# Optimization experiments

Hardware: AMD Instinct MI355X
Metric: run time of the kernel (lower is better)

## Reference

```python
import jax, jax.numpy as jnp
import numpy as np

DIM = 768
NUM_HEADS = 12
HEAD_DIM = DIM // NUM_HEADS
SCALE = HEAD_DIM ** -0.5


def setup_inputs() -> dict:
    key = jax.random.key(0)
    k_x, k_qw, k_qb, k_pw, k_pb = jax.random.split(key, 5)
    B, S = 4, 2048
    x = jax.random.normal(k_x, (B, S, DIM), dtype=jnp.float32)
    # torch nn.Linear convention: weight shape [out_features, in_features]
    qkv_w = jax.random.normal(k_qw, (2 * DIM, DIM), dtype=jnp.float32) * 0.02
    qkv_b = jax.random.normal(k_qb, (2 * DIM,), dtype=jnp.float32) * 0.02
    proj_w = jax.random.normal(k_pw, (DIM, DIM), dtype=jnp.float32) * 0.02
    proj_b = jax.random.normal(k_pb, (DIM,), dtype=jnp.float32) * 0.02
    return {"x": x, "qkv_w": qkv_w, "qkv_b": qkv_b, "proj_w": proj_w, "proj_b": proj_b}


def reference(x, qkv_w, qkv_b, proj_w, proj_b):
    B, S, D = x.shape
    H, Hd = NUM_HEADS, HEAD_DIM
    # qkv projection -> (B, S, 2*D)
    qkv = jnp.einsum('bsd,ed->bse', x, qkv_w) + qkv_b
    # reshape to (B, S, 2, H, Hd) then split q, v with heads leading: (B, H, S, Hd)
    qkv = qkv.reshape(B, S, 2, H, Hd).transpose(2, 0, 3, 1, 4)
    q, v = qkv[0], qkv[1]
    q = q * SCALE
    # shared Q=K scores: (B, H, S, S)
    attn = jnp.einsum('bhid,bhjd->bhij', q, q)
    attn = jax.nn.softmax(attn, axis=-1)  # attn_drop p=0 (identity)
    out = jnp.einsum('bhij,bhjd->bhid', attn, v)
    out = out.transpose(0, 2, 1, 3).reshape(B, S, D)
    out = jnp.einsum('bsd,ed->bse', out, proj_w) + proj_b  # proj_drop p=0
    return out
```

## Files before the change

kernel.cpp:

```cpp
#include <hip/hip_runtime.h>
#include <hip/hip_bf16.h>

#define NH 12
#define HD 64
#define SEQ 2048
#define DM 768

typedef __attribute__((ext_vector_type(8))) short bf16x8;
typedef __attribute__((ext_vector_type(4))) short bf16x4;
typedef __attribute__((ext_vector_type(4))) float f32x4;

static __device__ __forceinline__ unsigned short f2bf(float f) {
  unsigned int u = __float_as_uint(f);
  u += 0x7fff + ((u >> 16) & 1);
  return (unsigned short)(u >> 16);
}

static __device__ __forceinline__ unsigned cvt_pk_bf16(float lo, float hi) {
  unsigned r;
  asm("v_cvt_pk_bf16_f32 %0, %1, %2" : "=v"(r) : "v"(lo), "v"(hi));
  return r;
}

static __device__ __forceinline__ void gload_lds16(const void* g, void* l) {
  __builtin_amdgcn_global_load_lds(
      (const __attribute__((address_space(1))) void*)g,
      (__attribute__((address_space(3))) void*)l, 16, 0, 0);
}

#define QSCALE 0.15014030f

__global__ __launch_bounds__(256) void cvt3_kernel(
    const float* __restrict__ s0, unsigned short* __restrict__ d0, int n0,
    const float* __restrict__ s1, unsigned short* __restrict__ d1, int n1,
    const float* __restrict__ s2, unsigned short* __restrict__ d2, int n2) {
  int i = blockIdx.x * 256 + threadIdx.x;
  const int stride = gridDim.x * 256;
  const int ntot = n0 + n1 + n2;
  for (; i < ntot; i += stride) {
    const float* src;
    unsigned short* dst;
    int j = i;
    if (j < n0) { src = s0; dst = d0; }
    else if (j < n0 + n1) { j -= n0; src = s1; dst = d1; }
    else { j -= n0 + n1; src = s2; dst = d2; }
    const float4 a = reinterpret_cast<const float4*>(src)[j * 2];
    const float4 b = reinterpret_cast<const float4*>(src)[j * 2 + 1];
    ushort4 lo = make_ushort4(f2bf(a.x), f2bf(a.y), f2bf(a.z), f2bf(a.w));
    ushort4 hi = make_ushort4(f2bf(b.x), f2bf(b.y), f2bf(b.z), f2bf(b.w));
    reinterpret_cast<ushort4*>(dst)[j * 2] = lo;
    reinterpret_cast<ushort4*>(dst)[j * 2 + 1] = hi;
  }
}

__global__ __launch_bounds__(256) void qkv_kernel(
    const unsigned short* __restrict__ xb, const unsigned short* __restrict__ wb,
    const float* __restrict__ bias,
    unsigned short* __restrict__ qb, unsigned short* __restrict__ vtb) {
  __shared__ alignas(16) char As[2][8192];
  __shared__ alignas(16) char Bs[2][8192];
  const int tid = threadIdx.x;
  const int lane = tid & 63, wid = tid >> 6;
  const int wr = wid >> 1, wc = wid & 1;
  const int g = lane >> 4, c = lane & 15;
  const int m0 = blockIdx.x * 128, n0 = blockIdx.y * 128;
  const char* Ab = (const char*)xb;
  const char* Bb = (const char*)wb;

  const int o0 = tid * 16, o1 = tid * 16 + 4096;
  const int r0 = o0 >> 6, r1 = o1 >> 6;
  const int sw0 = (o0 & 63) ^ (((r0 >> 1) & 3) << 4);
  const int sw1 = (o1 & 63) ^ (((r1 >> 1) & 3) << 4);

  auto stage = [&](int kt, int buf) {
    const int k0b = kt * 64;
    gload_lds16(Ab + (size_t)(m0 + r0) * 1536 + k0b + sw0, &As[buf][o0]);
    gload_lds16(Bb + (size_t)(n0 + r0) * 1536 + k0b + sw0, &Bs[buf][o0]);
    gload_lds16(Ab + (size_t)(m0 + r1) * 1536 + k0b + sw1, &As[buf][o1]);
    gload_lds16(Bb + (size_t)(n0 + r1) * 1536 + k0b + sw1, &Bs[buf][o1]);
  };

  f32x4 acc[4][4] = {};
  stage(0, 0);

  for (int kt = 0; kt < 24; ++kt) {
    __syncthreads();
    if (kt < 23) stage(kt + 1, (kt + 1) & 1);
    const char* Ap = As[kt & 1];
    const char* Bp = Bs[kt & 1];
    bf16x8 a_f[4], b_f[4];
#pragma unroll
    for (int i = 0; i < 4; ++i) {
      const int ra = wr * 64 + i * 16 + c;
      const int rb = wc * 64 + i * 16 + c;
      a_f[i] = *reinterpret_cast<const bf16x8*>(Ap + ra * 64 + ((g ^ ((ra >> 1) & 3)) << 4));
      b_f[i] = *reinterpret_cast<const bf16x8*>(Bp + rb * 64 + ((g ^ ((rb >> 1) & 3)) << 4));
    }
#pragma unroll
    for (int ai = 0; ai < 4; ++ai)
#pragma unroll
      for (int ni = 0; ni < 4; ++ni)
        acc[ai][ni] = __builtin_amdgcn_mfma_f32_16x16x32_bf16(a_f[ai], b_f[ni], acc[ai][ni], 0, 0, 0);
  }

#pragma unroll
  for (int ni = 0; ni < 4; ++ni) {
    const int n = n0 + wc * 64 + ni * 16 + c;
    const float bn = bias[n];
    if (n < DM) {
      const int h = n >> 6, d = n & 63;
#pragma unroll
      for (int ai = 0; ai < 4; ++ai)
#pragma unroll
        for (int r = 0; r < 4; ++r) {
          const int m = m0 + wr * 64 + ai * 16 + g * 4 + r;
          const int bb = m >> 11, s = m & 2047;
          qb[(((size_t)(bb * NH + h)) * SEQ + s) * HD + d] = f2bf((acc[ai][ni][r] + bn) * QSCALE);
        }
    } else {
      const int nn = n - DM;
      const int h = nn >> 6, d = nn & 63;
#pragma unroll
      for (int ai = 0; ai < 4; ++ai) {
        const int m_base = m0 + wr * 64 + ai * 16 + g * 4;
        const int bb = m_base >> 11, s0 = m_base & 2047;
        const int blk = s0 >> 5, off = s0 & 31;
        const int offp = (((off >> 4) & 1) << 2) + (((off >> 2) & 3) << 3);
        ushort4 pk = make_ushort4(f2bf(acc[ai][ni][0] + bn), f2bf(acc[ai][ni][1] + bn),
                                  f2bf(acc[ai][ni][2] + bn), f2bf(acc[ai][ni][3] + bn));
        *reinterpret_cast<ushort4*>(
            &vtb[((size_t)(bb * NH + h) * HD + d) * SEQ + blk * 32 + offp]) = pk;
      }
    }
  }
}

__global__ __launch_bounds__(256, 5) void attn_kernel(
    const unsigned short* __restrict__ qb, const unsigned short* __restrict__ vtb,
    unsigned short* __restrict__ ao) {
  __shared__ alignas(16) char pool[2][16384];

  const int tid = threadIdx.x;
  const int lane = tid & 63, wid = tid >> 6;
  const int g = lane >> 4, c = lane & 15;
  const int wq = wid >> 1, wk = wid & 1;

  const int wg = blockIdx.x;
  const int xcd = wg & 7;
  const int idx = wg >> 3;
  const int bh = xcd * 6 + (idx >> 5);
  const int qs0 = (idx & 31) * 64;
  const size_t base = (size_t)bh * SEQ * HD;

  bf16x8 qf[2][2];
#pragma unroll
  for (int jq = 0; jq < 2; ++jq) {
    const unsigned short* qrow = &qb[base + (size_t)(qs0 + wq * 32 + jq * 16 + c) * HD + g * 8];
    qf[jq][0] = *reinterpret_cast<const bf16x8*>(qrow);
    qf[jq][1] = *reinterpret_cast<const bf16x8*>(qrow + 32);
  }

  const char* qbB = (const char*)qb;
  const char* vtB = (const char*)vtb;
  const int oK0 = tid * 16, oK1 = tid * 16 + 4096;
  const int swK0 = oK0 ^ (((oK0 >> 7) & 7) << 4);
  const int swK1 = oK1 ^ (((oK1 >> 7) & 7) << 4);
  const int rV0 = oK0 >> 7, rV1 = oK1 >> 7;
  const int swV0 = (oK0 & 127) ^ ((rV0 & 7) << 4);
  const int swV1 = (oK1 & 127) ^ ((rV1 & 7) << 4);

  auto stage = [&](int t, int buf) {
    char* P = pool[buf];
    const size_t kQ = base * 2 + (size_t)t * 8192;
    gload_lds16(qbB + kQ + swK0, P + oK0);
    gload_lds16(qbB + kQ + swK1, P + oK1);
    gload_lds16(vtB + ((size_t)(bh * HD + rV0) * SEQ + t * 64) * 2 + swV0, P + 8192 + oK0);
    gload_lds16(vtB + ((size_t)(bh * HD + rV1) * SEQ + t * 64) * 2 + swV1, P + 8192 + oK1);
  };

  float l_p[2] = {0.f, 0.f};
  f32x4 o_acc[4][2] = {};

  const int cswz = (c & 7) << 4;

  stage(0, 0);
  asm volatile("s_waitcnt vmcnt(0)" ::: "memory");
  __builtin_amdgcn_sched_barrier(0);
  __builtin_amdgcn_s_barrier();

  for (int t = 0; t < 32; ++t) {
    const char* P = pool[t & 1];
    if (t < 31) stage(t + 1, (t + 1) & 1);

    f32x4 sa[2][2] = {};
    __builtin_amdgcn_s_setprio(1);
#pragma unroll
    for (int jp = 0; jp < 2; ++jp) {
      const int krow = wk * 32 + jp * 16 + c;
      const bf16x8 kf0 = *reinterpret_cast<const bf16x8*>(P + krow * 128 + ((g * 16) ^ cswz));
      const bf16x8 kf1 = *reinterpret_cast<const bf16x8*>(P + krow * 128 + ((64 + g * 16) ^ cswz));
#pragma unroll
      for (int jq = 0; jq < 2; ++jq) {
        sa[jp][jq] = __builtin_amdgcn_mfma_f32_16x16x32_bf16(kf0, qf[jq][0], sa[jp][jq], 0, 0, 0);
        sa[jp][jq] = __builtin_amdgcn_mfma_f32_16x16x32_bf16(kf1, qf[jq][1], sa[jp][jq], 0, 0, 0);
      }
    }
    __builtin_amdgcn_s_setprio(0);

    bf16x8 pvv[2];
#pragma unroll
    for (int jq = 0; jq < 2; ++jq) {
      float a0 = __builtin_amdgcn_exp2f(sa[0][jq][0]);
      float a1 = __builtin_amdgcn_exp2f(sa[0][jq][1]);
      float a2 = __builtin_amdgcn_exp2f(sa[0][jq][2]);
      float a3 = __builtin_amdgcn_exp2f(sa[0][jq][3]);
      float b0 = __builtin_amdgcn_exp2f(sa[1][jq][0]);
      float b1 = __builtin_amdgcn_exp2f(sa[1][jq][1]);
      float b2 = __builtin_amdgcn_exp2f(sa[1][jq][2]);
      float b3 = __builtin_amdgcn_exp2f(sa[1][jq][3]);
      l_p[jq] += ((a0 + a1) + (a2 + a3)) + ((b0 + b1) + (b2 + b3));
      uint4 u = make_uint4(cvt_pk_bf16(a0, a1), cvt_pk_bf16(a2, a3),
                           cvt_pk_bf16(b0, b1), cvt_pk_bf16(b2, b3));
      pvv[jq] = *reinterpret_cast<bf16x8*>(&u);
    }

    __builtin_amdgcn_s_setprio(1);
#pragma unroll
    for (int dn = 0; dn < 4; ++dn) {
      const int vrow = dn * 16 + c;
      const bf16x8 av = *reinterpret_cast<const bf16x8*>(
          P + 8192 + vrow * 128 + ((wk * 64 + 16 * g) ^ ((vrow & 7) << 4)));
#pragma unroll
      for (int jq = 0; jq < 2; ++jq)
        o_acc[dn][jq] = __builtin_amdgcn_mfma_f32_16x16x32_bf16(av, pvv[jq], o_acc[dn][jq], 0, 0, 0);
    }
    __builtin_amdgcn_s_setprio(0);

    asm volatile("s_waitcnt vmcnt(0)" ::: "memory");
    __builtin_amdgcn_sched_barrier(0);
    __builtin_amdgcn_s_barrier();
  }

#pragma unroll
  for (int jq = 0; jq < 2; ++jq) {
    float v = l_p[jq];
    v += __shfl_xor(v, 16);
    v += __shfl_xor(v, 32);
    l_p[jq] = v;
  }

  float* ex = (float*)(pool[0] + wq * 16384);
  float* exl = ex + 32 * 68;
  if (wk == 1) {
#pragma unroll
    for (int dn = 0; dn < 4; ++dn)
#pragma unroll
      for (int jq = 0; jq < 2; ++jq)
        *reinterpret_cast<f32x4*>(&ex[(jq * 16 + c) * 68 + dn * 16 + 4 * g]) = o_acc[dn][jq];
    if (g == 0) {
      exl[c] = l_p[0];
      exl[16 + c] = l_p[1];
    }
  }
  __syncthreads();
  if (wk == 0) {
    const int b = bh / NH, h = bh % NH;
    float linv[2];
#pragma unroll
    for (int jq = 0; jq < 2; ++jq)
      linv[jq] = __builtin_amdgcn_rcpf(l_p[jq] + exl[jq * 16 + c]);
#pragma unroll
    for (int dn = 0; dn < 4; ++dn)
#pragma unroll
      for (int jq = 0; jq < 2; ++jq) {
        f32x4 o = o_acc[dn][jq];
        o += *reinterpret_cast<const f32x4*>(&ex[(jq * 16 + c) * 68 + dn * 16 + 4 * g]);
        uint2 wv = make_uint2(cvt_pk_bf16(o[0] * linv[jq], o[1] * linv[jq]),
                              cvt_pk_bf16(o[2] * linv[jq], o[3] * linv[jq]));
        *reinterpret_cast<uint2*>(
            &ao[((size_t)b * SEQ + qs0 + wq * 32 + jq * 16 + c) * DM + h * HD + dn * 16 + 4 * g]) = wv;
      }
  }
}

__global__ __launch_bounds__(256) void proj_kernel(
    const unsigned short* __restrict__ ao, const unsigned short* __restrict__ pwb,
    const float* __restrict__ bias, float* __restrict__ out) {
  __shared__ alignas(16) char As[2][4096];
  __shared__ alignas(16) char Bs[2][8192];
  const int tid = threadIdx.x;
  const int lane = tid & 63, wid = tid >> 6;
  const int g = lane >> 4, c = lane & 15;
  const int m0 = blockIdx.x * 64, n0 = blockIdx.y * 128;
  const char* Ab = (const char*)ao;
  const char* Bb = (const char*)pwb;

  const int oA = tid * 16;
  const int rA = oA >> 6;
  const int swA = (oA & 63) ^ (((rA >> 1) & 3) << 4);
  const int oB0 = tid * 16, oB1 = tid * 16 + 4096;
  const int rB0 = oB0 >> 6, rB1 = oB1 >> 6;
  const int swB0 = (oB0 & 63) ^ (((rB0 >> 1) & 3) << 4);
  const int swB1 = (oB1 & 63) ^ (((rB1 >> 1) & 3) << 4);

  auto stage = [&](int kt, int buf) {
    const int k0b = kt * 64;
    gload_lds16(Ab + (size_t)(m0 + rA) * 1536 + k0b + swA, &As[buf][oA]);
    gload_lds16(Bb + (size_t)(n0 + rB0) * 1536 + k0b + swB0, &Bs[buf][oB0]);
    gload_lds16(Bb + (size_t)(n0 + rB1) * 1536 + k0b + swB1, &Bs[buf][oB1]);
  };

  f32x4 acc[4][2] = {};
  stage(0, 0);

  for (int kt = 0; kt < 24; ++kt) {
    __syncthreads();
    if (kt < 23) stage(kt + 1, (kt + 1) & 1);
    const char* Ap = As[kt & 1];
    const char* Bp = Bs[kt & 1];
    bf16x8 a_f[4], b_f[2];
#pragma unroll
    for (int i = 0; i < 4; ++i) {
      const int ra = i * 16 + c;
      a_f[i] = *reinterpret_cast<const bf16x8*>(Ap + ra * 64 + ((g ^ ((ra >> 1) & 3)) << 4));
    }
#pragma unroll
    for (int j = 0; j < 2; ++j) {
      const int rb = wid * 32 + j * 16 + c;
      b_f[j] = *reinterpret_cast<const bf16x8*>(Bp + rb * 64 + ((g ^ ((rb >> 1) & 3)) << 4));
    }
#pragma unroll
    for (int i = 0; i < 4; ++i)
#pragma unroll
      for (int j = 0; j < 2; ++j)
        acc[i][j] = __builtin_amdgcn_mfma_f32_16x16x32_bf16(a_f[i], b_f[j], acc[i][j], 0, 0, 0);
  }

#pragma unroll
  for (int j = 0; j < 2; ++j) {
    const int n = n0 + wid * 32 + j * 16 + c;
    const float bn = bias[n];
#pragma unroll
    for (int i = 0; i < 4; ++i)
#pragma unroll
      for (int r = 0; r < 4; ++r) {
        const int m = m0 + i * 16 + g * 4 + r;
        out[(size_t)m * DM + n] = acc[i][j][r] + bn;
      }
  }
}

extern "C" void kernel_launch(void* const* d_in, const int* in_sizes, int n_in,
                              void* d_out, int out_size, void* d_ws, size_t ws_size,
                              hipStream_t stream) {
  const float* x = (const float*)d_in[0];
  const float* qkv_w = (const float*)d_in[1];
  const float* qkv_b = (const float*)d_in[2];
  const float* proj_w = (const float*)d_in[3];
  const float* proj_b = (const float*)d_in[4];
  float* out = (float*)d_out;

  const size_t elems = (size_t)4 * NH * SEQ * HD;
  unsigned short* qbuf = (unsigned short*)d_ws;
  unsigned short* vtbuf = qbuf + elems;
  unsigned short* xbf = vtbuf + elems;
  unsigned short* aobuf = xbf;
  unsigned short* wqkvbf = xbf + elems;
  unsigned short* wprojbf = wqkvbf + (size_t)2 * DM * DM;

  cvt3_kernel<<<dim3(2048), 256, 0, stream>>>(
      x, xbf, (int)(elems / 8),
      qkv_w, wqkvbf, 2 * DM * DM / 8,
      proj_w, wprojbf, DM * DM / 8);

  qkv_kernel<<<dim3(64, 12), 256, 0, stream>>>(xbf, wqkvbf, qkv_b, qbuf, vtbuf);
  attn_kernel<<<dim3(1536), 256, 0, stream>>>(qbuf, vtbuf, aobuf);
  proj_kernel<<<dim3(128, 6), 256, 0, stream>>>(aobuf, wprojbf, proj_b, out);
}
```

Baseline: 123.1 us.

## Double K-tile depth in QKV/proj GEMMs, remap blocks per XCD, relax attn bounds

The QKV and projection GEMMs now stage 128-wide K tiles with a new 8-way XOR swizzle, halving the number of barrier-separated iterations and issuing two MFMAs per accumulator per step. Blocks are launched on a 1-D grid and remapped so each XCD handles a contiguous group of M rows, aiming for better L2 reuse of the input rows. The attention kernel's launch-bounds occupancy hint drops from 5 to 4 waves, giving the compiler more registers. LDS use per GEMM block doubles, which may lower occupancy.

```diff
diff --git a/kernel.cpp b/kernel.cpp
--- a/kernel.cpp
+++ b/kernel.cpp
@@ -57,50 +57,60 @@
     const unsigned short* __restrict__ xb, const unsigned short* __restrict__ wb,
     const float* __restrict__ bias,
     unsigned short* __restrict__ qb, unsigned short* __restrict__ vtb) {
-  __shared__ alignas(16) char As[2][8192];
-  __shared__ alignas(16) char Bs[2][8192];
+  __shared__ alignas(16) char As[2][16384];
+  __shared__ alignas(16) char Bs[2][16384];
   const int tid = threadIdx.x;
   const int lane = tid & 63, wid = tid >> 6;
   const int wr = wid >> 1, wc = wid & 1;
   const int g = lane >> 4, c = lane & 15;
-  const int m0 = blockIdx.x * 128, n0 = blockIdx.y * 128;
+
+  const int wg = blockIdx.x;
+  const int xcd = wg & 7;
+  const int idx = wg >> 3;
+  const int m0 = (xcd * 8 + (idx & 7)) * 128;
+  const int n0 = (idx >> 3) * 128;
   const char* Ab = (const char*)xb;
   const char* Bb = (const char*)wb;
 
-  const int o0 = tid * 16, o1 = tid * 16 + 4096;
-  const int r0 = o0 >> 6, r1 = o1 >> 6;
-  const int sw0 = (o0 & 63) ^ (((r0 >> 1) & 3) << 4);
-  const int sw1 = (o1 & 63) ^ (((r1 >> 1) & 3) << 4);
-
   auto stage = [&](int kt, int buf) {
-    const int k0b = kt * 64;
-    gload_lds16(Ab + (size_t)(m0 + r0) * 1536 + k0b + sw0, &As[buf][o0]);
-    gload_lds16(Bb + (size_t)(n0 + r0) * 1536 + k0b + sw0, &Bs[buf][o0]);
-    gload_lds16(Ab + (size_t)(m0 + r1) * 1536 + k0b + sw1, &As[buf][o1]);
-    gload_lds16(Bb + (size_t)(n0 + r1) * 1536 + k0b + sw1, &Bs[buf][o1]);
+    const int k0b = kt * 128;
+#pragma unroll
+    for (int i = 0; i < 4; ++i) {
+      const int o = tid * 16 + i * 4096;
+      const int row = o >> 7;
+      const int colb = (o & 127) ^ ((row & 7) << 4);
+      gload_lds16(Ab + (size_t)(m0 + row) * 1536 + k0b + colb, &As[buf][o]);
+      gload_lds16(Bb + (size_t)(n0 + row) * 1536 + k0b + colb, &Bs[buf][o]);
+    }
   };
 
   f32x4 acc[4][4] = {};
   stage(0, 0);
 
-  for (int kt = 0; kt < 24; ++kt) {
+  for (int kt = 0; kt < 12; ++kt) {
     __syncthreads();
-    if (kt < 23) stage(kt + 1, (kt + 1) & 1);
+    if (kt < 11) stage(kt + 1, (kt + 1) & 1);
     const char* Ap = As[kt & 1];
     const char* Bp = Bs[kt & 1];
-    bf16x8 a_f[4], b_f[4];
+    bf16x8 a_f[4][2], b_f[4][2];
 #pragma unroll
     for (int i = 0; i < 4; ++i) {
       const int ra = wr * 64 + i * 16 + c;
       const int rb = wc * 64 + i * 16 + c;
-      a_f[i] = *reinterpret_cast<const bf16x8*>(Ap + ra * 64 + ((g ^ ((ra >> 1) & 3)) << 4));
-      b_f[i] = *reinterpret_cast<const bf16x8*>(Bp + rb * 64 + ((g ^ ((rb >> 1) & 3)) << 4));
+      const int sa = (ra & 7) << 4, sb = (rb & 7) << 4;
+#pragma unroll
+      for (int ks = 0; ks < 2; ++ks) {
+        a_f[i][ks] = *reinterpret_cast<const bf16x8*>(Ap + ra * 128 + ((ks * 64 + g * 16) ^ sa));
+        b_f[i][ks] = *reinterpret_cast<const bf16x8*>(Bp + rb * 128 + ((ks * 64 + g * 16) ^ sb));
+      }
     }
 #pragma unroll
     for (int ai = 0; ai < 4; ++ai)
 #pragma unroll
-      for (int ni = 0; ni < 4; ++ni)
-        acc[ai][ni] = __builtin_amdgcn_mfma_f32_16x16x32_bf16(a_f[ai], b_f[ni], acc[ai][ni], 0, 0, 0);
+      for (int ni = 0; ni < 4; ++ni) {
+        acc[ai][ni] = __builtin_amdgcn_mfma_f32_16x16x32_bf16(a_f[ai][0], b_f[ni][0], acc[ai][ni], 0, 0, 0);
+        acc[ai][ni] = __builtin_amdgcn_mfma_f32_16x16x32_bf16(a_f[ai][1], b_f[ni][1], acc[ai][ni], 0, 0, 0);
+      }
   }
 
 #pragma unroll
@@ -135,7 +145,7 @@
   }
 }
 
-__global__ __launch_bounds__(256, 5) void attn_kernel(
+__global__ __launch_bounds__(256, 4) void attn_kernel(
     const unsigned short* __restrict__ qb, const unsigned short* __restrict__ vtb,
     unsigned short* __restrict__ ao) {
   __shared__ alignas(16) char pool[2][16384];
@@ -286,54 +296,70 @@
 __global__ __launch_bounds__(256) void proj_kernel(
     const unsigned short* __restrict__ ao, const unsigned short* __restrict__ pwb,
     const float* __restrict__ bias, float* __restrict__ out) {
-  __shared__ alignas(16) char As[2][4096];
-  __shared__ alignas(16) char Bs[2][8192];
+  __shared__ alignas(16) char As[2][8192];
+  __shared__ alignas(16) char Bs[2][16384];
   const int tid = threadIdx.x;
   const int lane = tid & 63, wid = tid >> 6;
   const int g = lane >> 4, c = lane & 15;
-  const int m0 = blockIdx.x * 64, n0 = blockIdx.y * 128;
+
+  const int wg = blockIdx.x;
+  const int xcd = wg & 7;
+  const int idx = wg >> 3;
+  const int m0 = (xcd * 16 + (idx & 15)) * 64;
+  const int n0 = (idx >> 4) * 128;
   const char* Ab = (const char*)ao;
   const char* Bb = (const char*)pwb;
 
-  const int oA = tid * 16;
-  const int rA = oA >> 6;
-  const int swA = (oA & 63) ^ (((rA >> 1) & 3) << 4);
-  const int oB0 = tid * 16, oB1 = tid * 16 + 4096;
-  const int rB0 = oB0 >> 6, rB1 = oB1 >> 6;
-  const int swB0 = (oB0 & 63) ^ (((rB0 >> 1) & 3) << 4);
-  const int swB1 = (oB1 & 63) ^ (((rB1 >> 1) & 3) << 4);
-
   auto stage = [&](int kt, int buf) {
-    const int k0b = kt * 64;
-    gload_lds16(Ab + (size_t)(m0 + rA) * 1536 + k0b + swA, &As[buf][oA]);
-    gload_lds16(Bb + (size_t)(n0 + rB0) * 1536 + k0b + swB0, &Bs[buf][oB0]);
-    gload_lds16(Bb + (size_t)(n0 + rB1) * 1536 + k0b + swB1, &Bs[buf][oB1]);
+    const int k0b = kt * 128;
+#pragma unroll
+    for (int i = 0; i < 2; ++i) {
+      const int o = tid * 16 + i * 4096;
+      const int row = o >> 7;
+      const int colb = (o & 127) ^ ((row & 7) << 4);
+      gload_lds16(Ab + (size_t)(m0 + row) * 1536 + k0b + colb, &As[buf][o]);
+    }
+#pragma unroll
+    for (int i = 0; i < 4; ++i) {
+      const int o = tid * 16 + i * 4096;
+      const int row = o >> 7;
+      const int colb = (o & 127) ^ ((row & 7) << 4);
+      gload_lds16(Bb + (size_t)(n0 + row) * 1536 + k0b + colb, &Bs[buf][o]);
+    }
   };
 
   f32x4 acc[4][2] = {};
   stage(0, 0);
 
-  for (int kt = 0; kt < 24; ++kt) {
+  for (int kt = 0; kt < 12; ++kt) {
     __syncthreads();
-    if (kt < 23) stage(kt + 1, (kt + 1) & 1);
+    if (kt < 11) stage(kt + 1, (kt + 1) & 1);
     const char* Ap = As[kt & 1];
     const char* Bp = Bs[kt & 1];
-    bf16x8 a_f[4], b_f[2];
+    bf16x8 a_f[4][2], b_f[2][2];
 #pragma unroll
     for (int i = 0; i < 4; ++i) {
       const int ra = i * 16 + c;
-      a_f[i] = *reinterpret_cast<const bf16x8*>(Ap + ra * 64 + ((g ^ ((ra >> 1) & 3)) << 4));
+      const int sa = (ra & 7) << 4;
+#pragma unroll
+      for (int ks = 0; ks < 2; ++ks)
+        a_f[i][ks] = *reinterpret_cast<const bf16x8*>(Ap + ra * 128 + ((ks * 64 + g * 16) ^ sa));
     }
 #pragma unroll
     for (int j = 0; j < 2; ++j) {
       const int rb = wid * 32 + j * 16 + c;
-      b_f[j] = *reinterpret_cast<const bf16x8*>(Bp + rb * 64 + ((g ^ ((rb >> 1) & 3)) << 4));
+      const int sb = (rb & 7) << 4;
+#pragma unroll
+      for (int ks = 0; ks < 2; ++ks)
+        b_f[j][ks] = *reinterpret_cast<const bf16x8*>(Bp + rb * 128 + ((ks * 64 + g * 16) ^ sb));
     }
 #pragma unroll
     for (int i = 0; i < 4; ++i)
 #pragma unroll
-      for (int j = 0; j < 2; ++j)
-        acc[i][j] = __builtin_amdgcn_mfma_f32_16x16x32_bf16(a_f[i], b_f[j], acc[i][j], 0, 0, 0);
+      for (int j = 0; j < 2; ++j) {
+        acc[i][j] = __builtin_amdgcn_mfma_f32_16x16x32_bf16(a_f[i][0], b_f[j][0], acc[i][j], 0, 0, 0);
+        acc[i][j] = __builtin_amdgcn_mfma_f32_16x16x32_bf16(a_f[i][1], b_f[j][1], acc[i][j], 0, 0, 0);
+      }
   }
 
 #pragma unroll
@@ -373,7 +399,7 @@
       qkv_w, wqkvbf, 2 * DM * DM / 8,
       proj_w, wprojbf, DM * DM / 8);
 
-  qkv_kernel<<<dim3(64, 12), 256, 0, stream>>>(xbf, wqkvbf, qkv_b, qbuf, vtbuf);
+  qkv_kernel<<<dim3(768), 256, 0, stream>>>(xbf, wqkvbf, qkv_b, qbuf, vtbuf);
   attn_kernel<<<dim3(1536), 256, 0, stream>>>(qbuf, vtbuf, aobuf);
-  proj_kernel<<<dim3(128, 6), 256, 0, stream>>>(aobuf, wprojbf, proj_b, out);
-}
+  proj_kernel<<<dim3(768), 256, 0, stream>>>(aobuf, wprojbf, proj_b, out);
+}
```

After: 116.4 us, median of 2. 1.06x faster.
